# Optimization experiments

Measured on AMD Instinct MI355X. Metric: run time of the kernel, lower is better.

## Reference

```python
import jax, jax.numpy as jnp
import numpy as np

T, B, IN = 256, 64, 512
HIDDEN = [512, 512, 512]
DILATIONS = [1, 2, 4]


def _lstm_scan(x, W_ih, W_hh, b_ih, b_hh):
    """Run an LSTMCell over leading time axis of x: [Td, N, D] -> [Td, N, H]."""
    H = W_hh.shape[1]
    N = x.shape[1]
    h0 = jnp.zeros((N, H), x.dtype)
    c0 = jnp.zeros((N, H), x.dtype)

    def step(carry, xt):
        h, c = carry
        gates = xt @ W_ih.T + b_ih + h @ W_hh.T + b_hh  # [N, 4H], torch order i,f,g,o
        i, f, g, o = jnp.split(gates, 4, axis=-1)
        c = jax.nn.sigmoid(f) * c + jax.nn.sigmoid(i) * jnp.tanh(g)
        h = jax.nn.sigmoid(o) * jnp.tanh(c)
        return (h, c), h

    _, hs = jax.lax.scan(step, (h0, c0), x)
    return hs


def _drnn_layer(x, rate, W_ih, W_hh, b_ih, b_hh):
    """Dilated RNN layer. x: [T, B, D] with T % rate == 0.
    Torch code concats `rate` consecutive timesteps along batch -> one dilated step;
    reshape [T,B,D] -> [T//rate, rate*B, D] reproduces exactly that layout, and the
    chunk/unroll at the end is the inverse reshape."""
    Tn, Bn, D = x.shape
    Td = Tn // rate
    xd = x.reshape(Td, rate * Bn, D)
    hs = _lstm_scan(xd, W_ih, W_hh, b_ih, b_hh)  # [Td, rate*B, H]
    return hs.reshape(Tn, Bn, W_hh.shape[1])


def setup_inputs() -> dict:
    key = jax.random.key(0)
    ks = jax.random.split(key, 1 + 4 * len(HIDDEN))
    inp = {"x": jax.random.normal(ks[0], (T, B, IN), dtype=jnp.float32)}
    in_dim = IN
    ki = 1
    for li, H in enumerate(HIDDEN):
        bound = 1.0 / np.sqrt(H)
        inp[f"W_ih{li}"] = jax.random.uniform(ks[ki + 0], (4 * H, in_dim), jnp.float32, -bound, bound)
        inp[f"W_hh{li}"] = jax.random.uniform(ks[ki + 1], (4 * H, H), jnp.float32, -bound, bound)
        inp[f"b_ih{li}"] = jax.random.uniform(ks[ki + 2], (4 * H,), jnp.float32, -bound, bound)
        inp[f"b_hh{li}"] = jax.random.uniform(ks[ki + 3], (4 * H,), jnp.float32, -bound, bound)
        ki += 4
        in_dim = H
    return inp


def reference(x,
              W_ih0, W_hh0, b_ih0, b_hh0,
              W_ih1, W_hh1, b_ih1, b_hh1,
              W_ih2, W_hh2, b_ih2, b_hh2):
    params = [(W_ih0, W_hh0, b_ih0, b_hh0),
              (W_ih1, W_hh1, b_ih1, b_hh1),
              (W_ih2, W_hh2, b_ih2, b_hh2)]
    h = x
    for (Wih, Whh, bih, bhh), rate in zip(params, DILATIONS):
        h = _drnn_layer(h, rate, Wih, Whh, bih, bhh)
    return h  # [T, B, HIDDEN[-1]]
```

## Files before the change

kernel.cpp:

```cpp
#include <hip/hip_runtime.h>

typedef __attribute__((ext_vector_type(8))) short bf16x8;
typedef __attribute__((ext_vector_type(4))) float f32x4;

__device__ __forceinline__ unsigned short f2bf(float x) {
    unsigned u = __float_as_uint(x);
    u += 0x7FFFu + ((u >> 16) & 1u);
    return (unsigned short)(u >> 16);
}
__device__ __forceinline__ float sigm(float x) { return 1.0f / (1.0f + __expf(-x)); }
__device__ __forceinline__ float ftanh(float x) {
    float e = __expf(2.f * x);
    return 1.f - 2.f / (e + 1.f);
}

__device__ __forceinline__ void gld16(const unsigned short* g, unsigned short* l) {
    __builtin_amdgcn_global_load_lds((const __attribute__((address_space(1))) void*)g,
                                     (__attribute__((address_space(3))) void*)l, 16, 0, 0);
}

__device__ __forceinline__ void st_plain32(unsigned* p, unsigned v) {
    asm volatile("global_store_dword %0, %1, off" :: "v"(p), "v"(v) : "memory");
}
__device__ __forceinline__ void st_wt32(unsigned* p, unsigned v) {
    asm volatile("global_store_dword %0, %1, off sc0 sc1" :: "v"(p), "v"(v) : "memory");
}
__device__ __forceinline__ void aaddMALL(unsigned* p) {
    unsigned one = 1;
    asm volatile("global_atomic_add %0, %1, off sc1" :: "v"(p), "v"(one) : "memory");
}
__device__ __forceinline__ unsigned ld_mall(const unsigned* p) {
    unsigned v;
    asm volatile("global_load_dword %0, %1, off sc0 sc1\n\ts_waitcnt vmcnt(0)"
                 : "=v"(v) : "v"(p) : "memory");
    return v;
}
__device__ __forceinline__ void st_wt16(unsigned short* p, unsigned v) {
    asm volatile("global_store_short %0, %1, off sc0 sc1" :: "v"(p), "v"(v) : "memory");
}

__device__ __forceinline__ float dppx1(float x) {
    return __int_as_float(__builtin_amdgcn_mov_dpp(__float_as_int(x), 0xB1, 0xF, 0xF, true));
}
__device__ __forceinline__ float dppx2(float x) {
    return __int_as_float(__builtin_amdgcn_mov_dpp(__float_as_int(x), 0x4E, 0xF, 0xF, true));
}

__global__ __launch_bounds__(256) void k_conv_x(const float* __restrict__ x,
                                                unsigned short* __restrict__ Xp) {
    int i = blockIdx.x * 256 + threadIdx.x;
    int rb = i >> 10, kc = (i >> 6) & 15, ln = i & 63;
    int row = (rb << 4) + (ln & 15);
    int k   = (kc << 5) + ((ln >> 4) << 3);
    const float* s = x + (size_t)row * 512 + k;
    float4 v0 = *(const float4*)s, v1 = *(const float4*)(s + 4);
    unsigned short o[8] = {f2bf(v0.x), f2bf(v0.y), f2bf(v0.z), f2bf(v0.w),
                           f2bf(v1.x), f2bf(v1.y), f2bf(v1.z), f2bf(v1.w)};
    *(bf16x8*)(Xp + (size_t)i * 8) = *(bf16x8*)o;
}

__global__ __launch_bounds__(256) void k_conv_w(const float* __restrict__ Wih,
                                                const float* __restrict__ Whh,
                                                unsigned short* __restrict__ Wp) {
    int i = blockIdx.x * 256 + threadIdx.x;
    int wrb = i >> 11, kc = (i >> 6) & 31, ln = i & 63;
    int j = (wrb << 4) + (ln & 15);
    int k = (kc << 5) + ((ln >> 4) << 3);
    int srow = (j & 3) * 512 + (j >> 2);
    const float* s = (k < 512) ? (Wih + (size_t)srow * 512 + k)
                               : (Whh + (size_t)srow * 512 + (k - 512));
    float4 v0 = *(const float4*)s, v1 = *(const float4*)(s + 4);
    unsigned short o[8] = {f2bf(v0.x), f2bf(v0.y), f2bf(v0.z), f2bf(v0.w),
                           f2bf(v1.x), f2bf(v1.y), f2bf(v1.z), f2bf(v1.w)};
    *(bf16x8*)(Wp + (size_t)i * 8) = *(bf16x8*)o;
}

struct DP {
    const unsigned short* Xp;
    unsigned short *Hp0, *Hp1, *Hp2;
    unsigned short *Xq1, *Xq2;
    const unsigned short *Wp0, *Wp1, *Wp2;
    const float *bi0, *bh0, *bi1, *bh1, *bi2, *bh2;
    float* Out;
    unsigned int* flags;
};

__device__ __forceinline__ void quadT(f32x4 a, int sq, float& G0, float& G1, float& G2, float& G3) {
    float a0 = a[0], a1 = a[1], a2 = a[2], a3 = a[3];
    float p1 = (sq & 1) ? a0 : a1; float g1_ = dppx1(p1);
    float p2 = (sq & 1) ? a2 : a3; float g2_ = dppx1(p2);
    float m0 = (sq & 1) ? g1_ : a0, m1 = (sq & 1) ? a1 : g1_;
    float m2 = (sq & 1) ? g2_ : a2, m3 = (sq & 1) ? a3 : g2_;
    float q1 = (sq & 2) ? m0 : m2; float h1_ = dppx2(q1);
    float q2 = (sq & 2) ? m1 : m3; float h2_ = dppx2(q2);
    G0 = (sq & 2) ? h1_ : m0; G1 = (sq & 2) ? h2_ : m1;
    G2 = (sq & 2) ? m2 : h1_; G3 = (sq & 2) ? m3 : h2_;
}

#define PIN8(A,B,C,D,E,F,G,H) \
    asm volatile("" : "+v"(A),"+v"(B),"+v"(C),"+v"(D),"+v"(E),"+v"(F),"+v"(G),"+v"(H))
#define SBAR()  __builtin_amdgcn_sched_barrier(0)
#define MEMBAR() asm volatile("" ::: "memory")
#define RAWBAR() do { MEMBAR(); SBAR(); __builtin_amdgcn_s_barrier(); SBAR(); MEMBAR(); } while (0)

__global__ __launch_bounds__(256, 1) void k_drnn(DP p) {
    const int tid = threadIdx.x, lane = tid & 63, wv = tid >> 6;
    const int l15 = lane & 15, lhi = lane >> 4, sq = l15 & 3;

    const int b = blockIdx.x;
    const int cid = b & 7, w = b >> 3;
    int l, c, T, P, N;
    if (cid < 2)      { l = 0; c = cid;     T = 256; P = 1; N = 64;  }
    else if (cid < 4) { l = 1; c = cid - 2; T = 128; P = 2; N = 128; }
    else              { l = 2; c = cid - 4; T = 64;  P = 2; N = 256; }

    const unsigned short* Xs = (l == 0) ? p.Xp  : (l == 1 ? p.Xq1 : p.Xq2);
    unsigned short*       Hd = (l == 0) ? p.Hp0 : (l == 1 ? p.Hp1 : p.Hp2);
    unsigned short*       Xw = (l == 0) ? p.Xq1 : (l == 1 ? p.Xq2 : nullptr);
    const unsigned short* Ws = (l == 0) ? p.Wp0 : (l == 1 ? p.Wp1 : p.Wp2);
    const float* bi = (l == 0) ? p.bi0 : (l == 1 ? p.bi1 : p.bi2);
    const float* bh = (l == 0) ? p.bh0 : (l == 1 ? p.bh1 : p.bh2);
    const int R0 = c * (P * 32);
    const int alias = (p.Xq1 == p.Hp0);

    __shared__ unsigned short At[65536];
    __shared__ unsigned pollbuf[32];

    const unsigned short* wbase = Ws + ((size_t)(((w << 2) + wv) * 32) << 9) + lane * 8;
#define DECLW(n) bf16x8 w##n = *(const bf16x8*)(wbase + (n << 9));
    DECLW(0) DECLW(1) DECLW(2) DECLW(3) DECLW(4) DECLW(5) DECLW(6) DECLW(7)
    DECLW(8) DECLW(9) DECLW(10) DECLW(11) DECLW(12) DECLW(13) DECLW(14) DECLW(15)
    DECLW(16) DECLW(17) DECLW(18) DECLW(19) DECLW(20) DECLW(21) DECLW(22) DECLW(23)
    DECLW(24) DECLW(25) DECLW(26) DECLW(27) DECLW(28) DECLW(29) DECLW(30) DECLW(31)

    const int hcol = (w << 4) + (wv << 2) + (l15 >> 2);
    const float bs0 = bi[hcol]        + bh[hcol];
    const float bs1 = bi[512 + hcol]  + bh[512 + hcol];
    const float bs2 = bi[1024 + hcol] + bh[1024 + hcol];
    const float bs3 = bi[1536 + hcol] + bh[1536 + hcol];

    const int kch = hcol >> 5;
    const int lane16 = (((hcol & 31) >> 3) << 4) + ((lhi << 2) + sq);
    const int st_lt = lane16 * 8 + (hcol & 7);

    float cst0 = 0.f, cst1 = 0.f, cst2 = 0.f, cst3 = 0.f;
    unsigned int* iflagV = p.flags;
    unsigned int* mflagV = p.flags + 256;
    unsigned int* cflagS = p.flags + 512;
    int fastok = 1;

#define KPn(na, nb) { \
    bf16x8 xa = *(const bf16x8*)(a0 + ((na) << 9)); \
    bf16x8 xb = *(const bf16x8*)(a1 + ((na) << 9)); \
    bf16x8 ya = *(const bf16x8*)(a0 + ((nb) << 9)); \
    bf16x8 yb = *(const bf16x8*)(a1 + ((nb) << 9)); \
    e0 = __builtin_amdgcn_mfma_f32_16x16x32_bf16(xa, w##na, e0, 0, 0, 0); \
    e1 = __builtin_amdgcn_mfma_f32_16x16x32_bf16(xb, w##na, e1, 0, 0, 0); \
    o0 = __builtin_amdgcn_mfma_f32_16x16x32_bf16(ya, w##nb, o0, 0, 0, 0); \
    o1 = __builtin_amdgcn_mfma_f32_16x16x32_bf16(yb, w##nb, o1, 0, 0, 0); }

#define PWC(RV, CSTV, HV) { \
    float G0, G1, G2, G3; quadT(RV, sq, G0, G1, G2, G3); \
    float cn = sigm(G1 + bs1) * CSTV + sigm(G0 + bs0) * ftanh(G2 + bs2); \
    HV = sigm(G3 + bs3) * ftanh(cn); CSTV = cn; }

#define DOPASS(PI, CA, CB, HA, HB) { \
    const unsigned short* a0 = At + (((PI) * 64) << 9) + lane * 8; \
    const unsigned short* a1 = a0 + (32 << 9); \
    f32x4 e0 = {0.f,0.f,0.f,0.f}, o0 = {0.f,0.f,0.f,0.f}; \
    f32x4 e1 = {0.f,0.f,0.f,0.f}, o1 = {0.f,0.f,0.f,0.f}; \
    KPn(0,1) KPn(2,3) KPn(4,5) KPn(6,7) KPn(8,9) KPn(10,11) KPn(12,13) KPn(14,15) \
    KPn(16,17) KPn(18,19) KPn(20,21) KPn(22,23) KPn(24,25) KPn(26,27) KPn(28,29) KPn(30,31) \
    f32x4 r0 = e0 + o0, r1 = e1 + o1; \
    PWC(r0, CA, HA) PWC(r1, CB, HB) }

    for (int t = 0; t < T; ++t) {
        PIN8(w0,w1,w2,w3,w4,w5,w6,w7);
        PIN8(w8,w9,w10,w11,w12,w13,w14,w15);
        PIN8(w16,w17,w18,w19,w20,w21,w22,w23);
        PIN8(w24,w25,w26,w27,w28,w29,w30,w31);

        const int RxB = (t * N + R0) >> 4;

        if (l == 0 && wv < 2) {
            #pragma unroll
            for (int i = 0; i < 16; ++i) {
                int q = (wv << 4) + i, rb = q >> 4, kc = q & 15;
                gld16(Xs + ((size_t)((RxB + rb) * 16 + kc) << 9) + lane * 8,
                      &At[(rb * 32 + kc) << 9]);
            }
        }

        if (wv == 0 && t > 0) {
            const unsigned need = (unsigned)t;
            const unsigned* mp = mflagV + cid * 32 + (lane & 31);
            if (t == T - 1 || !fastok) {
                int n = 0;
                while (!__all(ld_mall(mp) >= need)) { if (++n > (1 << 22)) break; }
            } else {
                const unsigned short* gip = (const unsigned short*)(iflagV + cid * 32);
                volatile unsigned* pb = pollbuf;
                int n = 0;
                for (;;) {
                    if (lane < 8) gld16(gip + lane * 8, (unsigned short*)pollbuf);
                    asm volatile("s_waitcnt vmcnt(0)" ::: "memory");
                    SBAR();
                    unsigned v = pb[lane & 31];
                    if (__all((v - need) <= 1u)) break;
                    if (++n > 1024) {
                        fastok = 0;
                        int m = 0;
                        while (!__all(ld_mall(mp) >= need)) { if (++m > (1 << 22)) break; }
                        break;
                    }
                }
            }
        }
        if (l == 1 && wv == 1 && lane < 2) {
            const unsigned* cp = cflagS + lane * 32;
            const unsigned need = 32u * (unsigned)(2 * t + c + 1);
            int n = 0;
            while (!__all(ld_mall(cp) >= need)) { if (++n > (1 << 22)) break; }
        }
        if (l == 2 && wv == 1 && lane == 0) {
            const unsigned* cp = cflagS + (2 + (c & 1)) * 32;
            const unsigned need = 32u * (unsigned)(2 * t + (c >> 1) + 1);
            int n = 0;
            while (ld_mall(cp) < need) { if (++n > (1 << 22)) break; }
        }
        if (wv < 2) asm volatile("s_waitcnt vmcnt(0)" ::: "memory");
        RAWBAR();

        float hv0, hv1, hv2 = 0.f, hv3 = 0.f;
        if (l == 0) {
            if (t > 0) {
                if (wv >= 2) {
                    const int RhB = ((t - 1) * N + R0) >> 4;
                    #pragma unroll
                    for (int i = 0; i < 16; ++i) {
                        int q = ((wv - 2) << 4) + i, rb = q >> 4, kc = q & 15;
                        gld16(Hd + ((size_t)((RhB + rb) * 16 + kc) << 9) + lane * 8,
                              &At[(rb * 32 + 16 + kc) << 9]);
                    }
                }
            } else {
                #pragma unroll
                for (int rb = 0; rb < 2; ++rb)
                    #pragma unroll
                    for (int it = 0; it < 4; ++it)
                        *(float4*)&At[((rb * 32 + 16) << 9) + (it * 256 + tid) * 8] =
                            (float4){0.f, 0.f, 0.f, 0.f};
            }
            SBAR();
            const unsigned short* a0 = At + lane * 8;
            const unsigned short* a1 = a0 + (32 << 9);
            f32x4 e0 = {0.f,0.f,0.f,0.f}, o0 = {0.f,0.f,0.f,0.f};
            f32x4 e1 = {0.f,0.f,0.f,0.f}, o1 = {0.f,0.f,0.f,0.f};
            KPn(0,1) KPn(2,3) KPn(4,5) KPn(6,7)
            KPn(8,9) KPn(10,11) KPn(12,13) KPn(14,15)
            if (wv >= 2) asm volatile("s_waitcnt vmcnt(0)" ::: "memory");
            asm volatile("s_waitcnt lgkmcnt(0)" ::: "memory");
            RAWBAR();
            KPn(16,17) KPn(18,19) KPn(20,21) KPn(22,23)
            KPn(24,25) KPn(26,27) KPn(28,29) KPn(30,31)
            f32x4 r0 = e0 + o0, r1 = e1 + o1;
            PWC(r0, cst0, hv0) PWC(r1, cst1, hv1)
        } else {
            if (wv < 2) {
                #pragma unroll
                for (int i = 0; i < 32; ++i) {
                    int q = (wv << 5) + i, rb = q >> 4, kc = q & 15;
                    gld16(Xs + ((size_t)((RxB + rb) * 16 + kc) << 9) + lane * 8,
                          &At[(rb * 32 + kc) << 9]);
                }
            }
            if (t > 0) {
                if (wv >= 2) {
                    const int RhB = ((t - 1) * N + R0) >> 4;
                    #pragma unroll
                    for (int i = 0; i < 32; ++i) {
                        int q = ((wv - 2) << 5) + i, rb = q >> 4, kc = q & 15;
                        gld16(Hd + ((size_t)((RhB + rb) * 16 + kc) << 9) + lane * 8,
                              &At[(rb * 32 + 16 + kc) << 9]);
                    }
                }
            } else {
                #pragma unroll
                for (int rb = 0; rb < 4; ++rb)
                    #pragma unroll
                    for (int it = 0; it < 4; ++it)
                        *(float4*)&At[((rb * 32 + 16) << 9) + (it * 256 + tid) * 8] =
                            (float4){0.f, 0.f, 0.f, 0.f};
            }
            asm volatile("s_waitcnt vmcnt(0)" ::: "memory");
            asm volatile("s_waitcnt lgkmcnt(0)" ::: "memory");
            RAWBAR();
            DOPASS(0, cst0, cst1, hv0, hv1)
            DOPASS(1, cst2, cst3, hv2, hv3)
        }

        const unsigned short hb0 = f2bf(hv0), hb1 = f2bf(hv1);
        const unsigned short hb2 = f2bf(hv2), hb3 = f2bf(hv3);
        const size_t i0 = ((size_t)((RxB + 0) * 16 + kch) << 9) + st_lt;
        const size_t i1 = ((size_t)((RxB + 1) * 16 + kch) << 9) + st_lt;
        const size_t i2 = ((size_t)((RxB + 2) * 16 + kch) << 9) + st_lt;
        const size_t i3 = ((size_t)((RxB + 3) * 16 + kch) << 9) + st_lt;
        if (!alias || l == 2) {
            Hd[i0] = hb0; Hd[i1] = hb1;
            if (P == 2) { Hd[i2] = hb2; Hd[i3] = hb3; }
        }
        if (l == 2) {
            p.Out[((size_t)(((RxB + 0) << 4) + (lhi << 2) + sq)) * 512 + hcol] = hv0;
            p.Out[((size_t)(((RxB + 1) << 4) + (lhi << 2) + sq)) * 512 + hcol] = hv1;
            p.Out[((size_t)(((RxB + 2) << 4) + (lhi << 2) + sq)) * 512 + hcol] = hv2;
            p.Out[((size_t)(((RxB + 3) << 4) + (lhi << 2) + sq)) * 512 + hcol] = hv3;
        }
        MEMBAR(); SBAR();
        if (l == 0) { st_wt16(Xw + i0, hb0); st_wt16(Xw + i1, hb1); }
        else if (l == 1) { st_wt16(Xw + i0, hb0); st_wt16(Xw + i1, hb1);
                           st_wt16(Xw + i2, hb2); st_wt16(Xw + i3, hb3); }
        SBAR();
        if (alias && l < 2)  asm volatile("s_waitcnt vmcnt(0)" ::: "memory");
        else if (l == 0)     asm volatile("s_waitcnt vmcnt(2)" ::: "memory");
        else                 asm volatile("s_waitcnt vmcnt(4)" ::: "memory");
        RAWBAR();
        if (tid == 192) {
            st_plain32(iflagV + cid * 32 + w, (unsigned)(t + 1));
            st_wt32(mflagV + cid * 32 + w, (unsigned)(t + 1));
        }
        if (tid == 128 && l < 2 && t > 0) aaddMALL(cflagS + cid * 32);
    }

    asm volatile("s_waitcnt vmcnt(0)" ::: "memory");
    __builtin_amdgcn_s_barrier();
    if (tid == 128 && l < 2) aaddMALL(cflagS + cid * 32);
}

extern "C" void kernel_launch(void* const* d_in, const int* in_sizes, int n_in,
                              void* d_out, int out_size, void* d_ws, size_t ws_size,
                              hipStream_t stream)
{
    const float* x = (const float*)d_in[0];
    const float* Wih[3] = {(const float*)d_in[1], (const float*)d_in[5], (const float*)d_in[9]};
    const float* Whh[3] = {(const float*)d_in[2], (const float*)d_in[6], (const float*)d_in[10]};
    const float* bih[3] = {(const float*)d_in[3], (const float*)d_in[7], (const float*)d_in[11]};
    const float* bhh[3] = {(const float*)d_in[4], (const float*)d_in[8], (const float*)d_in[12]};

    char* wp = (char*)d_ws;
    const size_t SZ_A = (size_t)16384 * 512;
    unsigned int* flags = (unsigned int*)wp; wp += 4096;
    unsigned short* Xp  = (unsigned short*)wp; wp += SZ_A * 2;
    unsigned short* Hp0 = (unsigned short*)wp; wp += SZ_A * 2;
    unsigned short* Hp1 = (unsigned short*)wp; wp += SZ_A * 2;
    unsigned short* Hp2 = (unsigned short*)wp; wp += SZ_A * 2;
    unsigned short* Wp[3];
    for (int l = 0; l < 3; ++l) { Wp[l] = (unsigned short*)wp; wp += (size_t)2048 * 1024 * 2; }
    unsigned short* Xq1 = (unsigned short*)wp; wp += SZ_A * 2;
    unsigned short* Xq2 = (unsigned short*)wp; wp += SZ_A * 2;
    const size_t need = (size_t)(wp - (char*)d_ws);
    if (ws_size < need) { Xq1 = Hp0; Xq2 = Hp1; }

    hipMemsetAsync(flags, 0, 4096, stream);
    k_conv_x<<<dim3(4096), dim3(256), 0, stream>>>(x, Xp);
    for (int l = 0; l < 3; ++l)
        k_conv_w<<<dim3(1024), dim3(256), 0, stream>>>(Wih[l], Whh[l], Wp[l]);

    DP dp;
    dp.Xp = Xp; dp.Hp0 = Hp0; dp.Hp1 = Hp1; dp.Hp2 = Hp2;
    dp.Xq1 = Xq1; dp.Xq2 = Xq2;
    dp.Wp0 = Wp[0]; dp.Wp1 = Wp[1]; dp.Wp2 = Wp[2];
    dp.bi0 = bih[0]; dp.bh0 = bhh[0];
    dp.bi1 = bih[1]; dp.bh1 = bhh[1];
    dp.bi2 = bih[2]; dp.bh2 = bhh[2];
    dp.Out = (float*)d_out; dp.flags = flags;

    k_drnn<<<dim3(256), dim3(256), 0, stream>>>(dp);
}
```

Before: 951.5 us.

## Precompute next step's input projection before waiting on recurrent state

Restructures the persistent LSTM step loop so the input-projection MFMAs (x_t·W_ih) for step t+1 are staged and computed right after step t's output is published, before polling for the peer blocks' hidden-state flags. Only the W_hh·h part stays on the critical path after the inter-block wait. This aims to hide half the matmul latency behind the cross-block synchronization. It changes the order in which flags and counters are signalled, adds a final flag publish at loop exit, and keeps eight accumulators live, which raises register pressure.

```diff
diff --git a/kernel.cpp b/kernel.cpp
--- a/kernel.cpp
+++ b/kernel.cpp
@@ -149,30 +149,73 @@
     unsigned int* cflagS = p.flags + 512;
     int fastok = 1;
 
-#define KPn(na, nb) { \
-    bf16x8 xa = *(const bf16x8*)(a0 + ((na) << 9)); \
-    bf16x8 xb = *(const bf16x8*)(a1 + ((na) << 9)); \
-    bf16x8 ya = *(const bf16x8*)(a0 + ((nb) << 9)); \
-    bf16x8 yb = *(const bf16x8*)(a1 + ((nb) << 9)); \
-    e0 = __builtin_amdgcn_mfma_f32_16x16x32_bf16(xa, w##na, e0, 0, 0, 0); \
-    e1 = __builtin_amdgcn_mfma_f32_16x16x32_bf16(xb, w##na, e1, 0, 0, 0); \
-    o0 = __builtin_amdgcn_mfma_f32_16x16x32_bf16(ya, w##nb, o0, 0, 0, 0); \
-    o1 = __builtin_amdgcn_mfma_f32_16x16x32_bf16(yb, w##nb, o1, 0, 0, 0); }
+#define KPX(na, nb, E0, E1, O0, O1, A0, A1) { \
+    bf16x8 xa = *(const bf16x8*)((A0) + ((na) << 9)); \
+    bf16x8 xb = *(const bf16x8*)((A1) + ((na) << 9)); \
+    bf16x8 ya = *(const bf16x8*)((A0) + ((nb) << 9)); \
+    bf16x8 yb = *(const bf16x8*)((A1) + ((nb) << 9)); \
+    E0 = __builtin_amdgcn_mfma_f32_16x16x32_bf16(xa, w##na, E0, 0, 0, 0); \
+    E1 = __builtin_amdgcn_mfma_f32_16x16x32_bf16(xb, w##na, E1, 0, 0, 0); \
+    O0 = __builtin_amdgcn_mfma_f32_16x16x32_bf16(ya, w##nb, O0, 0, 0, 0); \
+    O1 = __builtin_amdgcn_mfma_f32_16x16x32_bf16(yb, w##nb, O1, 0, 0, 0); }
+
+#define XH(E0, E1, O0, O1, A0, A1) \
+    KPX(0,1,E0,E1,O0,O1,A0,A1) KPX(2,3,E0,E1,O0,O1,A0,A1) \
+    KPX(4,5,E0,E1,O0,O1,A0,A1) KPX(6,7,E0,E1,O0,O1,A0,A1) \
+    KPX(8,9,E0,E1,O0,O1,A0,A1) KPX(10,11,E0,E1,O0,O1,A0,A1) \
+    KPX(12,13,E0,E1,O0,O1,A0,A1) KPX(14,15,E0,E1,O0,O1,A0,A1)
+#define HH(E0, E1, O0, O1, A0, A1) \
+    KPX(16,17,E0,E1,O0,O1,A0,A1) KPX(18,19,E0,E1,O0,O1,A0,A1) \
+    KPX(20,21,E0,E1,O0,O1,A0,A1) KPX(22,23,E0,E1,O0,O1,A0,A1) \
+    KPX(24,25,E0,E1,O0,O1,A0,A1) KPX(26,27,E0,E1,O0,O1,A0,A1) \
+    KPX(28,29,E0,E1,O0,O1,A0,A1) KPX(30,31,E0,E1,O0,O1,A0,A1)
 
 #define PWC(RV, CSTV, HV) { \
     float G0, G1, G2, G3; quadT(RV, sq, G0, G1, G2, G3); \
     float cn = sigm(G1 + bs1) * CSTV + sigm(G0 + bs0) * ftanh(G2 + bs2); \
     HV = sigm(G3 + bs3) * ftanh(cn); CSTV = cn; }
 
-#define DOPASS(PI, CA, CB, HA, HB) { \
-    const unsigned short* a0 = At + (((PI) * 64) << 9) + lane * 8; \
-    const unsigned short* a1 = a0 + (32 << 9); \
-    f32x4 e0 = {0.f,0.f,0.f,0.f}, o0 = {0.f,0.f,0.f,0.f}; \
-    f32x4 e1 = {0.f,0.f,0.f,0.f}, o1 = {0.f,0.f,0.f,0.f}; \
-    KPn(0,1) KPn(2,3) KPn(4,5) KPn(6,7) KPn(8,9) KPn(10,11) KPn(12,13) KPn(14,15) \
-    KPn(16,17) KPn(18,19) KPn(20,21) KPn(22,23) KPn(24,25) KPn(26,27) KPn(28,29) KPn(30,31) \
-    f32x4 r0 = e0 + o0, r1 = e1 + o1; \
-    PWC(r0, CA, HA) PWC(r1, CB, HB) }
+#define STAGE_X(TT) { \
+    const int RxN = ((TT) * N + R0) >> 4; \
+    for (int i = 0; i < P * 8; ++i) { \
+        int q = wv * (P * 8) + i, rb = q >> 4, kc = q & 15; \
+        gld16(Xs + ((size_t)((RxN + rb) * 16 + kc) << 9) + lane * 8, \
+              &At[(rb * 32 + kc) << 9]); } }
+#define STAGE_H(TT) { \
+    const int RhN = ((TT) * N + R0) >> 4; \
+    for (int i = 0; i < P * 8; ++i) { \
+        int q = wv * (P * 8) + i, rb = q >> 4, kc = q & 15; \
+        gld16(Hd + ((size_t)((RhN + rb) * 16 + kc) << 9) + lane * 8, \
+              &At[(rb * 32 + 16 + kc) << 9]); } }
+
+#define CPOLL(TT) { \
+    if (l == 1 && wv == 1 && lane < 2) { \
+        const unsigned* cp = cflagS + lane * 32; \
+        const unsigned need = 32u * (unsigned)(2 * (TT) + c + 1); \
+        int n = 0; \
+        while (!__all(ld_mall(cp) >= need)) { if (++n > (1 << 22)) break; } \
+    } \
+    if (l == 2 && wv == 1 && lane == 0) { \
+        const unsigned* cp = cflagS + (2 + (c & 1)) * 32; \
+        const unsigned need = 32u * (unsigned)(2 * (TT) + (c >> 1) + 1); \
+        int n = 0; \
+        while (ld_mall(cp) < need) { if (++n > (1 << 22)) break; } \
+    } }
+
+    f32x4 e0 = {0,0,0,0}, e1 = {0,0,0,0}, o0 = {0,0,0,0}, o1 = {0,0,0,0};
+    f32x4 e2 = {0,0,0,0}, e3 = {0,0,0,0}, o2 = {0,0,0,0}, o3 = {0,0,0,0};
+    const unsigned short* A00 = At + lane * 8;
+    const unsigned short* A01 = A00 + (32 << 9);
+    const unsigned short* A10 = A00 + (64 << 9);
+    const unsigned short* A11 = A00 + (96 << 9);
+
+    if (l > 0) CPOLL(0);
+    RAWBAR();
+    STAGE_X(0);
+    asm volatile("s_waitcnt vmcnt(0)" ::: "memory");
+    RAWBAR();
+    { XH(e0, e1, o0, o1, A00, A01) }
+    if (P == 2) { XH(e2, e3, o2, o3, A10, A11) }
 
     for (int t = 0; t < T; ++t) {
         PIN8(w0,w1,w2,w3,w4,w5,w6,w7);
@@ -182,122 +225,46 @@
 
         const int RxB = (t * N + R0) >> 4;
 
-        if (l == 0 && wv < 2) {
-            #pragma unroll
-            for (int i = 0; i < 16; ++i) {
-                int q = (wv << 4) + i, rb = q >> 4, kc = q & 15;
-                gld16(Xs + ((size_t)((RxB + rb) * 16 + kc) << 9) + lane * 8,
-                      &At[(rb * 32 + kc) << 9]);
-            }
-        }
-
-        if (wv == 0 && t > 0) {
-            const unsigned need = (unsigned)t;
-            const unsigned* mp = mflagV + cid * 32 + (lane & 31);
-            if (t == T - 1 || !fastok) {
-                int n = 0;
-                while (!__all(ld_mall(mp) >= need)) { if (++n > (1 << 22)) break; }
-            } else {
-                const unsigned short* gip = (const unsigned short*)(iflagV + cid * 32);
-                volatile unsigned* pb = pollbuf;
-                int n = 0;
-                for (;;) {
-                    if (lane < 8) gld16(gip + lane * 8, (unsigned short*)pollbuf);
-                    asm volatile("s_waitcnt vmcnt(0)" ::: "memory");
-                    SBAR();
-                    unsigned v = pb[lane & 31];
-                    if (__all((v - need) <= 1u)) break;
-                    if (++n > 1024) {
-                        fastok = 0;
-                        int m = 0;
-                        while (!__all(ld_mall(mp) >= need)) { if (++m > (1 << 22)) break; }
-                        break;
+        if (t > 0) {
+            if (wv == 0) {
+                const unsigned need = (unsigned)t;
+                const unsigned* mp = mflagV + cid * 32 + (lane & 31);
+                if (t == T - 1 || !fastok) {
+                    int n = 0;
+                    while (!__all(ld_mall(mp) >= need)) { if (++n > (1 << 22)) break; }
+                } else {
+                    const unsigned short* gip = (const unsigned short*)(iflagV + cid * 32);
+                    volatile unsigned* pb = pollbuf;
+                    int n = 0;
+                    for (;;) {
+                        if (lane < 8) gld16(gip + lane * 8, (unsigned short*)pollbuf);
+                        asm volatile("s_waitcnt vmcnt(0)" ::: "memory");
+                        SBAR();
+                        unsigned v = pb[lane & 31];
+                        if (__all((v - need) <= 1u)) break;
+                        if (++n > 1024) {
+                            fastok = 0;
+                            int m = 0;
+                            while (!__all(ld_mall(mp) >= need)) { if (++m > (1 << 22)) break; }
+                            break;
+                        }
                     }
                 }
             }
+            RAWBAR();
+            STAGE_H(t - 1);
+            asm volatile("s_waitcnt vmcnt(0)" ::: "memory");
+            RAWBAR();
+            { HH(e0, e1, o0, o1, A00, A01) }
+            if (P == 2) { HH(e2, e3, o2, o3, A10, A11) }
         }
-        if (l == 1 && wv == 1 && lane < 2) {
-            const unsigned* cp = cflagS + lane * 32;
-            const unsigned need = 32u * (unsigned)(2 * t + c + 1);
-            int n = 0;
-            while (!__all(ld_mall(cp) >= need)) { if (++n > (1 << 22)) break; }
-        }
-        if (l == 2 && wv == 1 && lane == 0) {
-            const unsigned* cp = cflagS + (2 + (c & 1)) * 32;
-            const unsigned need = 32u * (unsigned)(2 * t + (c >> 1) + 1);
-            int n = 0;
-            while (ld_mall(cp) < need) { if (++n > (1 << 22)) break; }
-        }
-        if (wv < 2) asm volatile("s_waitcnt vmcnt(0)" ::: "memory");
-        RAWBAR();
 
         float hv0, hv1, hv2 = 0.f, hv3 = 0.f;
-        if (l == 0) {
-            if (t > 0) {
-                if (wv >= 2) {
-                    const int RhB = ((t - 1) * N + R0) >> 4;
-                    #pragma unroll
-                    for (int i = 0; i < 16; ++i) {
-                        int q = ((wv - 2) << 4) + i, rb = q >> 4, kc = q & 15;
-                        gld16(Hd + ((size_t)((RhB + rb) * 16 + kc) << 9) + lane * 8,
-                              &At[(rb * 32 + 16 + kc) << 9]);
-                    }
-                }
-            } else {
-                #pragma unroll
-                for (int rb = 0; rb < 2; ++rb)
-                    #pragma unroll
-                    for (int it = 0; it < 4; ++it)
-                        *(float4*)&At[((rb * 32 + 16) << 9) + (it * 256 + tid) * 8] =
-                            (float4){0.f, 0.f, 0.f, 0.f};
-            }
-            SBAR();
-            const unsigned short* a0 = At + lane * 8;
-            const unsigned short* a1 = a0 + (32 << 9);
-            f32x4 e0 = {0.f,0.f,0.f,0.f}, o0 = {0.f,0.f,0.f,0.f};
-            f32x4 e1 = {0.f,0.f,0.f,0.f}, o1 = {0.f,0.f,0.f,0.f};
-            KPn(0,1) KPn(2,3) KPn(4,5) KPn(6,7)
-            KPn(8,9) KPn(10,11) KPn(12,13) KPn(14,15)
-            if (wv >= 2) asm volatile("s_waitcnt vmcnt(0)" ::: "memory");
-            asm volatile("s_waitcnt lgkmcnt(0)" ::: "memory");
-            RAWBAR();
-            KPn(16,17) KPn(18,19) KPn(20,21) KPn(22,23)
-            KPn(24,25) KPn(26,27) KPn(28,29) KPn(30,31)
-            f32x4 r0 = e0 + o0, r1 = e1 + o1;
-            PWC(r0, cst0, hv0) PWC(r1, cst1, hv1)
-        } else {
-            if (wv < 2) {
-                #pragma unroll
-                for (int i = 0; i < 32; ++i) {
-                    int q = (wv << 5) + i, rb = q >> 4, kc = q & 15;
-                    gld16(Xs + ((size_t)((RxB + rb) * 16 + kc) << 9) + lane * 8,
-                          &At[(rb * 32 + kc) << 9]);
-                }
-            }
-            if (t > 0) {
-                if (wv >= 2) {
-                    const int RhB = ((t - 1) * N + R0) >> 4;
-                    #pragma unroll
-                    for (int i = 0; i < 32; ++i) {
-                        int q = ((wv - 2) << 5) + i, rb = q >> 4, kc = q & 15;
-                        gld16(Hd + ((size_t)((RhB + rb) * 16 + kc) << 9) + lane * 8,
-                              &At[(rb * 32 + 16 + kc) << 9]);
-                    }
-                }
-            } else {
-                #pragma unroll
-                for (int rb = 0; rb < 4; ++rb)
-                    #pragma unroll
-                    for (int it = 0; it < 4; ++it)
-                        *(float4*)&At[((rb * 32 + 16) << 9) + (it * 256 + tid) * 8] =
-                            (float4){0.f, 0.f, 0.f, 0.f};
-            }
-            asm volatile("s_waitcnt vmcnt(0)" ::: "memory");
-            asm volatile("s_waitcnt lgkmcnt(0)" ::: "memory");
-            RAWBAR();
-            DOPASS(0, cst0, cst1, hv0, hv1)
-            DOPASS(1, cst2, cst3, hv2, hv3)
-        }
+        { f32x4 r0 = e0 + o0, r1 = e1 + o1;
+          PWC(r0, cst0, hv0) PWC(r1, cst1, hv1) }
+        if (P == 2) {
+          f32x4 r2 = e2 + o2, r3 = e3 + o3;
+          PWC(r2, cst2, hv2) PWC(r3, cst3, hv3) }
 
         const unsigned short hb0 = f2bf(hv0), hb1 = f2bf(hv1);
         const unsigned short hb2 = f2bf(hv2), hb3 = f2bf(hv3);
@@ -324,16 +291,53 @@
         else if (l == 0)     asm volatile("s_waitcnt vmcnt(2)" ::: "memory");
         else                 asm volatile("s_waitcnt vmcnt(4)" ::: "memory");
         RAWBAR();
-        if (tid == 192) {
-            st_plain32(iflagV + cid * 32 + w, (unsigned)(t + 1));
-            st_wt32(mflagV + cid * 32 + w, (unsigned)(t + 1));
+
+        if (t + 1 < T) {
+            if (l == 0) {
+                STAGE_X(t + 1);
+                MEMBAR(); SBAR();
+                if (tid == 192) {
+                    st_plain32(iflagV + cid * 32 + w, (unsigned)(t + 1));
+                    st_wt32(mflagV + cid * 32 + w, (unsigned)(t + 1));
+                }
+                if (tid == 128 && t > 0) aaddMALL(cflagS + cid * 32);
+                SBAR();
+                if (wv == 3)                asm volatile("s_waitcnt vmcnt(2)" ::: "memory");
+                else if (wv == 2 && t > 0)  asm volatile("s_waitcnt vmcnt(1)" ::: "memory");
+                else                        asm volatile("s_waitcnt vmcnt(0)" ::: "memory");
+            } else {
+                if (tid == 192) {
+                    st_plain32(iflagV + cid * 32 + w, (unsigned)(t + 1));
+                    st_wt32(mflagV + cid * 32 + w, (unsigned)(t + 1));
+                }
+                if (tid == 128 && l == 1 && t > 0) aaddMALL(cflagS + cid * 32);
+                CPOLL(t + 1);
+                RAWBAR();
+                STAGE_X(t + 1);
+                asm volatile("s_waitcnt vmcnt(0)" ::: "memory");
+            }
+            RAWBAR();
+            e0 = (f32x4){0,0,0,0}; e1 = (f32x4){0,0,0,0};
+            o0 = (f32x4){0,0,0,0}; o1 = (f32x4){0,0,0,0};
+            { XH(e0, e1, o0, o1, A00, A01) }
+            if (P == 2) {
+                e2 = (f32x4){0,0,0,0}; e3 = (f32x4){0,0,0,0};
+                o2 = (f32x4){0,0,0,0}; o3 = (f32x4){0,0,0,0};
+                XH(e2, e3, o2, o3, A10, A11)
+            }
         }
-        if (tid == 128 && l < 2 && t > 0) aaddMALL(cflagS + cid * 32);
     }
 
     asm volatile("s_waitcnt vmcnt(0)" ::: "memory");
     __builtin_amdgcn_s_barrier();
-    if (tid == 128 && l < 2) aaddMALL(cflagS + cid * 32);
+    if (tid == 192) {
+        st_plain32(iflagV + cid * 32 + w, (unsigned)T);
+        st_wt32(mflagV + cid * 32 + w, (unsigned)T);
+    }
+    if (tid == 128 && l < 2) {
+        aaddMALL(cflagS + cid * 32);
+        aaddMALL(cflagS + cid * 32);
+    }
 }
 
 extern "C" void kernel_launch(void* const* d_in, const int* in_sizes, int n_in,
```

Result: no change. 934.2 us (-1.8%).
